# Performance work log

Measured on AMD Instinct MI355X. Metric: run time of the kernel, lower is better.

## Reference

```python
import jax, jax.numpy as jnp
import numpy as np

N_NODES = 50000
N_EDGES = 800000
IN_FEAT = 256
OUT_FEAT = 64
NHEAD = 4
ALPHA = 0.2  # LeakyReLU negative slope


def setup_inputs() -> dict:
    key = jax.random.key(0)
    k_x, k_e, k_w, k_al, k_ar = jax.random.split(key, 5)
    x = jax.random.normal(k_x, (N_NODES, IN_FEAT), dtype=jnp.float32)
    edge = jax.random.randint(k_e, (2, N_EDGES), 0, N_NODES, dtype=jnp.int64)
    # Glorot-uniform style init per reset_parameteres
    stdv_w = np.sqrt(6.0 / (IN_FEAT + OUT_FEAT * NHEAD))
    W = jax.random.uniform(k_w, (IN_FEAT, OUT_FEAT * NHEAD), minval=-stdv_w, maxval=stdv_w, dtype=jnp.float32)
    stdv_a = np.sqrt(6.0 / (NHEAD + OUT_FEAT))
    a_l = jax.random.uniform(k_al, (1, NHEAD, OUT_FEAT), minval=-stdv_a, maxval=stdv_a, dtype=jnp.float32)
    a_r = jax.random.uniform(k_ar, (1, NHEAD, OUT_FEAT), minval=-stdv_a, maxval=stdv_a, dtype=jnp.float32)
    return {"x": x, "edge": edge, "W": W, "a_l": a_l, "a_r": a_r}


def reference(x, edge, W, a_l, a_r):
    # x: [N, Fin], edge: [2, E], W: [Fin, H*F], a_l/a_r: [1, H, F]
    N = x.shape[0]
    H, F = a_l.shape[1], a_l.shape[2]
    h = (x @ W).reshape(N, H, F)                      # [N, H, F]
    h_l = (a_l * h).sum(-1)                            # [N, H]
    h_r = (a_r * h).sum(-1)                            # [N, H]
    row, col = edge[0], edge[1]                        # [E], [E]
    e = jax.nn.leaky_relu(h_l[row] + h_r[col], ALPHA)  # [E, H]
    # segment softmax over edges grouped by target node (row), per head
    m = jax.lax.stop_gradient(jax.ops.segment_max(e, row, num_segments=N))  # [N, H]
    ex = jnp.exp(e - m[row])                           # [E, H]
    denom = jax.ops.segment_sum(ex, row, num_segments=N)[row]  # [E, H]
    att = ex / jnp.maximum(denom, jnp.asarray(1e-16, ex.dtype))
    # spmm scatter-add: out[row] += att * h[col]  (dropout in eval mode = identity)
    msg = att[:, :, None] * h[col]                     # [E, H, F]
    out = jax.ops.segment_sum(msg, row, num_segments=N)  # [N, H, F]
    return out.reshape(N, H * F)                       # concat=True -> [N, H*F]
```

## Files before the change

kernel.cpp:

```cpp
#include <hip/hip_runtime.h>
#include <hip/hip_bf16.h>

#define N_FEAT 256
#define NHEAD 4
#define FDIM 64
#define ALPHA 0.2f

typedef __attribute__((ext_vector_type(8))) short frag8;
typedef __attribute__((ext_vector_type(4))) float f32x4;

static __device__ __forceinline__ unsigned short f2bf(float f) {
    __hip_bfloat16 b = __float2bfloat16(f);
    return *(unsigned short*)&b;
}
static __device__ __forceinline__ float bits2f(unsigned int u) {
    union { unsigned int u; float f; } cv; cv.u = u; return cv.f;
}

__global__ void transpose_w(const float* __restrict__ W, __hip_bfloat16* __restrict__ WT) {
    int n = blockIdx.x;
    int k = threadIdx.x;
    WT[n * 256 + k] = __float2bfloat16(W[k * 256 + n]);
}

__global__ __launch_bounds__(256) void gemm_mfma(const float* __restrict__ x,
                                                 const __hip_bfloat16* __restrict__ WT,
                                                 const float* __restrict__ a_l,
                                                 const float* __restrict__ a_r,
                                                 __hip_bfloat16* __restrict__ h2,
                                                 float* __restrict__ h_l,
                                                 float* __restrict__ h_r, int M) {
    __shared__ __hip_bfloat16 A[64][264];
    const int tid = threadIdx.x;
    const int wave = tid >> 6;
    const int lane = tid & 63;
    const int quad = lane >> 4;
    const int l16 = lane & 15;
    const int row0 = blockIdx.x * 64;

    {
        const int c4 = (tid & 63) * 4;
        const int rb = tid >> 6;
#pragma unroll 4
        for (int pass = 0; pass < 16; ++pass) {
            int r = pass * 4 + rb;
            int gr = row0 + r;
            float4 v = make_float4(0.f, 0.f, 0.f, 0.f);
            if (gr < M) v = *(const float4*)&x[(size_t)gr * 256 + c4];
            unsigned short s[4];
            s[0] = f2bf(v.x); s[1] = f2bf(v.y); s[2] = f2bf(v.z); s[3] = f2bf(v.w);
            *(ushort4*)&A[r][c4] = *(ushort4*)s;
        }
    }
    __syncthreads();

    f32x4 acc[4][4] = {};
    const int kq = quad * 8;
#pragma unroll
    for (int kk = 0; kk < 8; ++kk) {
        frag8 a[4], b[4];
#pragma unroll
        for (int tm = 0; tm < 4; ++tm)
            a[tm] = *(const frag8*)&A[tm * 16 + l16][kk * 32 + kq];
#pragma unroll
        for (int tn = 0; tn < 4; ++tn)
            b[tn] = *(const frag8*)&WT[(size_t)(wave * 64 + tn * 16 + l16) * 256 + kk * 32 + kq];
#pragma unroll
        for (int tm = 0; tm < 4; ++tm)
#pragma unroll
            for (int tn = 0; tn < 4; ++tn)
                acc[tm][tn] = __builtin_amdgcn_mfma_f32_16x16x32_bf16(a[tm], b[tn], acc[tm][tn], 0, 0, 0);
    }

#pragma unroll
    for (int tm = 0; tm < 4; ++tm) {
        int gr_base = row0 + tm * 16 + quad * 4;
#pragma unroll
        for (int tn = 0; tn < 4; ++tn) {
            int colg = wave * 64 + tn * 16 + l16;
#pragma unroll
            for (int reg = 0; reg < 4; ++reg) {
                int gr = gr_base + reg;
                if (gr < M)
                    h2[(size_t)gr * 256 + colg] = __float2bfloat16(acc[tm][tn][reg]);
            }
        }
    }

    float al[4], ar[4];
#pragma unroll
    for (int tn = 0; tn < 4; ++tn) {
        al[tn] = a_l[wave * 64 + tn * 16 + l16];
        ar[tn] = a_r[wave * 64 + tn * 16 + l16];
    }
#pragma unroll
    for (int tm = 0; tm < 4; ++tm) {
#pragma unroll
        for (int reg = 0; reg < 4; ++reg) {
            float vl = 0.f, vr = 0.f;
#pragma unroll
            for (int tn = 0; tn < 4; ++tn) {
                vl += acc[tm][tn][reg] * al[tn];
                vr += acc[tm][tn][reg] * ar[tn];
            }
#pragma unroll
            for (int m = 1; m < 16; m <<= 1) {
                vl += __shfl_xor(vl, m);
                vr += __shfl_xor(vr, m);
            }
            if (l16 == 0) {
                int gr = row0 + tm * 16 + quad * 4 + reg;
                if (gr < M) {
                    h_l[gr * NHEAD + wave] = vl;
                    h_r[gr * NHEAD + wave] = vr;
                }
            }
        }
    }
}

__global__ void hist_kernel(const int* __restrict__ row, int* __restrict__ deg,
                            int* __restrict__ rank, int E) {
    int e = blockIdx.x * blockDim.x + threadIdx.x;
    if (e < E) rank[e] = atomicAdd(&deg[row[e]], 1);
}

__global__ __launch_bounds__(256) void alloc_kernel(const int* __restrict__ deg,
                                                    int* __restrict__ row_ptr,
                                                    int* __restrict__ cursor, int N) {
    int i = blockIdx.x * blockDim.x + threadIdx.x;
    int lane = threadIdx.x & 63;
    int d = (i < N) ? deg[i] : 0;
    int pref = d;
#pragma unroll
    for (int off = 1; off < 64; off <<= 1) {
        int v = __shfl_up(pref, off);
        if (lane >= off) pref += v;
    }
    int total = __shfl(pref, 63);
    int base = 0;
    if (lane == 63) base = atomicAdd(cursor, total);
    base = __shfl(base, 63);
    if (i < N) row_ptr[i] = base + pref - d;
}

__global__ void scatter_kernel(const int* __restrict__ row, const int* __restrict__ col,
                               const int* __restrict__ row_ptr, const int* __restrict__ rank,
                               int* __restrict__ perm_col, int E) {
    int e = blockIdx.x * blockDim.x + threadIdx.x;
    if (e >= E) return;
    perm_col[row_ptr[row[e]] + rank[e]] = col[e];
}

__global__ __launch_bounds__(256) void aggregate_kernel(const __hip_bfloat16* __restrict__ h2,
                                                        const float* __restrict__ h_l,
                                                        const float* __restrict__ h_r,
                                                        const int* __restrict__ row_ptr,
                                                        const int* __restrict__ deg,
                                                        const int* __restrict__ perm_col,
                                                        float* __restrict__ out, int N) {
    int wave = threadIdx.x >> 6;
    int node = blockIdx.x * 4 + wave;
    if (node >= N) return;
    int lane = threadIdx.x & 63;
    int head = lane >> 4;
    int start = row_ptr[node];
    int end = start + deg[node];
    float hl = h_l[node * NHEAD + head];
    const float* hrh = h_r + head;
    const char* hbase = (const char*)h2 + (size_t)lane * 8;

    float4 acc = make_float4(0.f, 0.f, 0.f, 0.f);
    float s = 0.f;
    int j = start;
    for (; j + 4 <= end; j += 4) {
        int c0 = perm_col[j + 0];
        int c1 = perm_col[j + 1];
        int c2 = perm_col[j + 2];
        int c3 = perm_col[j + 3];
        uint2 g0 = *(const uint2*)(hbase + ((size_t)c0 << 9));
        uint2 g1 = *(const uint2*)(hbase + ((size_t)c1 << 9));
        uint2 g2 = *(const uint2*)(hbase + ((size_t)c2 << 9));
        uint2 g3 = *(const uint2*)(hbase + ((size_t)c3 << 9));
        float e0 = hl + hrh[c0 * NHEAD];
        float e1 = hl + hrh[c1 * NHEAD];
        float e2 = hl + hrh[c2 * NHEAD];
        float e3 = hl + hrh[c3 * NHEAD];
        e0 = fmaxf(e0, ALPHA * e0);
        e1 = fmaxf(e1, ALPHA * e1);
        e2 = fmaxf(e2, ALPHA * e2);
        e3 = fmaxf(e3, ALPHA * e3);
        float p0 = __expf(e0), p1 = __expf(e1), p2 = __expf(e2), p3 = __expf(e3);
        acc.x += p0 * bits2f(g0.x << 16);
        acc.y += p0 * bits2f(g0.x & 0xffff0000u);
        acc.z += p0 * bits2f(g0.y << 16);
        acc.w += p0 * bits2f(g0.y & 0xffff0000u);
        s += p0;
        acc.x += p1 * bits2f(g1.x << 16);
        acc.y += p1 * bits2f(g1.x & 0xffff0000u);
        acc.z += p1 * bits2f(g1.y << 16);
        acc.w += p1 * bits2f(g1.y & 0xffff0000u);
        s += p1;
        acc.x += p2 * bits2f(g2.x << 16);
        acc.y += p2 * bits2f(g2.x & 0xffff0000u);
        acc.z += p2 * bits2f(g2.y << 16);
        acc.w += p2 * bits2f(g2.y & 0xffff0000u);
        s += p2;
        acc.x += p3 * bits2f(g3.x << 16);
        acc.y += p3 * bits2f(g3.x & 0xffff0000u);
        acc.z += p3 * bits2f(g3.y << 16);
        acc.w += p3 * bits2f(g3.y & 0xffff0000u);
        s += p3;
    }
    for (; j < end; ++j) {
        int c = perm_col[j];
        uint2 g = *(const uint2*)(hbase + ((size_t)c << 9));
        float e = hl + hrh[c * NHEAD];
        e = fmaxf(e, ALPHA * e);
        float p = __expf(e);
        acc.x += p * bits2f(g.x << 16);
        acc.y += p * bits2f(g.x & 0xffff0000u);
        acc.z += p * bits2f(g.y << 16);
        acc.w += p * bits2f(g.y & 0xffff0000u);
        s += p;
    }
    float inv = 1.f / fmaxf(s, 1e-16f);
    acc.x *= inv; acc.y *= inv; acc.z *= inv; acc.w *= inv;
    *(float4*)&out[(size_t)node * N_FEAT + lane * 4] = acc;
}

extern "C" void kernel_launch(void* const* d_in, const int* in_sizes, int n_in,
                              void* d_out, int out_size, void* d_ws, size_t ws_size,
                              hipStream_t stream) {
    const float* x = (const float*)d_in[0];
    const int* edge = (const int*)d_in[1];
    const float* W = (const float*)d_in[2];
    const float* a_l = (const float*)d_in[3];
    const float* a_r = (const float*)d_in[4];
    float* out = (float*)d_out;

    const int N = in_sizes[0] / N_FEAT;
    const int E = in_sizes[1] / 2;
    const int* row = edge;
    const int* col = edge + E;

    char* p = (char*)d_ws;
    __hip_bfloat16* h2 = (__hip_bfloat16*)p; p += (size_t)N * N_FEAT * sizeof(__hip_bfloat16);
    __hip_bfloat16* WT = (__hip_bfloat16*)p; p += (size_t)256 * 256 * sizeof(__hip_bfloat16);
    float* h_l = (float*)p;      p += (size_t)N * NHEAD * sizeof(float);
    float* h_r = (float*)p;      p += (size_t)N * NHEAD * sizeof(float);
    int* deg = (int*)p;          p += (size_t)(N + 1) * sizeof(int);
    int* row_ptr = (int*)p;      p += (size_t)(N + 4) * sizeof(int);
    int* rank = (int*)p;         p += (size_t)E * sizeof(int);
    int* perm_col = (int*)p;     p += (size_t)E * sizeof(int);
    int* cursor = deg + N;

    hipMemsetAsync(deg, 0, (size_t)(N + 1) * sizeof(int), stream);

    transpose_w<<<256, 256, 0, stream>>>(W, WT);

    gemm_mfma<<<(N + 63) / 64, 256, 0, stream>>>(x, WT, a_l, a_r, h2, h_l, h_r, N);

    hist_kernel<<<(E + 255) / 256, 256, 0, stream>>>(row, deg, rank, E);
    alloc_kernel<<<(N + 255) / 256, 256, 0, stream>>>(deg, row_ptr, cursor, N);
    scatter_kernel<<<(E + 255) / 256, 256, 0, stream>>>(row, col, row_ptr, rank, perm_col, E);

    aggregate_kernel<<<(N + 3) / 4, 256, 0, stream>>>(h2, h_l, h_r, row_ptr, deg, perm_col, out, N);
}
```

Baseline: 270.4 us.

## Stage GEMM output through LDS, compute attention logits via MFMA, pad CSR rows

The GEMM now swaps MFMA operands so each lane holds contiguous output columns. It stages the bf16 result in shared memory and writes h2 with coalesced 16-byte stores instead of scattered 2-byte stores. The a_l/a_r dot products are computed with an extra MFMA on the staged bf16 tile rather than with shuffle reductions, which lowers the precision of the logits. CSR rows are padded to multiples of 4 so the aggregation loop can read column indices with 16-byte vector loads and unroll by 8, at the cost of a larger perm_col workspace.

After: 262.1 us. 3.1% less time.

```diff
diff --git a/kernel.cpp b/kernel.cpp
--- a/kernel.cpp
+++ b/kernel.cpp
@@ -58,62 +58,73 @@
     const int kq = quad * 8;
 #pragma unroll
     for (int kk = 0; kk < 8; ++kk) {
-        frag8 a[4], b[4];
+        frag8 xf[4], wf[4];
 #pragma unroll
         for (int tm = 0; tm < 4; ++tm)
-            a[tm] = *(const frag8*)&A[tm * 16 + l16][kk * 32 + kq];
+            xf[tm] = *(const frag8*)&A[tm * 16 + l16][kk * 32 + kq];
 #pragma unroll
         for (int tn = 0; tn < 4; ++tn)
-            b[tn] = *(const frag8*)&WT[(size_t)(wave * 64 + tn * 16 + l16) * 256 + kk * 32 + kq];
+            wf[tn] = *(const frag8*)&WT[(size_t)(wave * 64 + tn * 16 + l16) * 256 + kk * 32 + kq];
 #pragma unroll
         for (int tm = 0; tm < 4; ++tm)
 #pragma unroll
             for (int tn = 0; tn < 4; ++tn)
-                acc[tm][tn] = __builtin_amdgcn_mfma_f32_16x16x32_bf16(a[tm], b[tn], acc[tm][tn], 0, 0, 0);
-    }
-
+                acc[tm][tn] = __builtin_amdgcn_mfma_f32_16x16x32_bf16(wf[tn], xf[tm], acc[tm][tn], 0, 0, 0);
+    }
+
+    __syncthreads();
+
+#pragma unroll
+    for (int tm = 0; tm < 4; ++tm)
+#pragma unroll
+        for (int tn = 0; tn < 4; ++tn) {
+            unsigned short s4[4];
+            s4[0] = f2bf(acc[tm][tn][0]);
+            s4[1] = f2bf(acc[tm][tn][1]);
+            s4[2] = f2bf(acc[tm][tn][2]);
+            s4[3] = f2bf(acc[tm][tn][3]);
+            *(uint2*)&A[tm * 16 + l16][wave * 64 + tn * 16 + quad * 4] = *(uint2*)s4;
+        }
+    __syncthreads();
+
+    {
+        const int rsub = tid >> 5;
+        const int ce = (tid & 31) * 8;
+#pragma unroll
+        for (int pass = 0; pass < 8; ++pass) {
+            int r = pass * 8 + rsub;
+            int gr = row0 + r;
+            if (gr < M)
+                *(uint4*)&h2[(size_t)gr * 256 + ce] = *(const uint4*)&A[r][ce];
+        }
+    }
+
+    frag8 blr[2];
+#pragma unroll
+    for (int kk = 0; kk < 2; ++kk) {
+#pragma unroll
+        for (int j = 0; j < 8; ++j) {
+            float v = 0.f;
+            int f = wave * 64 + kk * 32 + quad * 8 + j;
+            if (l16 == 0) v = a_l[f];
+            else if (l16 == 1) v = a_r[f];
+            blr[kk][j] = (short)f2bf(v);
+        }
+    }
 #pragma unroll
     for (int tm = 0; tm < 4; ++tm) {
-        int gr_base = row0 + tm * 16 + quad * 4;
-#pragma unroll
-        for (int tn = 0; tn < 4; ++tn) {
-            int colg = wave * 64 + tn * 16 + l16;
-#pragma unroll
-            for (int reg = 0; reg < 4; ++reg) {
-                int gr = gr_base + reg;
-                if (gr < M)
-                    h2[(size_t)gr * 256 + colg] = __float2bfloat16(acc[tm][tn][reg]);
-            }
-        }
-    }
-
-    float al[4], ar[4];
-#pragma unroll
-    for (int tn = 0; tn < 4; ++tn) {
-        al[tn] = a_l[wave * 64 + tn * 16 + l16];
-        ar[tn] = a_r[wave * 64 + tn * 16 + l16];
-    }
-#pragma unroll
-    for (int tm = 0; tm < 4; ++tm) {
+        f32x4 dlr = {0.f, 0.f, 0.f, 0.f};
+#pragma unroll
+        for (int kk = 0; kk < 2; ++kk) {
+            frag8 ah = *(const frag8*)&A[tm * 16 + l16][wave * 64 + kk * 32 + quad * 8];
+            dlr = __builtin_amdgcn_mfma_f32_16x16x32_bf16(ah, blr[kk], dlr, 0, 0, 0);
+        }
 #pragma unroll
         for (int reg = 0; reg < 4; ++reg) {
-            float vl = 0.f, vr = 0.f;
-#pragma unroll
-            for (int tn = 0; tn < 4; ++tn) {
-                vl += acc[tm][tn][reg] * al[tn];
-                vr += acc[tm][tn][reg] * ar[tn];
-            }
-#pragma unroll
-            for (int m = 1; m < 16; m <<= 1) {
-                vl += __shfl_xor(vl, m);
-                vr += __shfl_xor(vr, m);
-            }
-            if (l16 == 0) {
-                int gr = row0 + tm * 16 + quad * 4 + reg;
-                if (gr < M) {
-                    h_l[gr * NHEAD + wave] = vl;
-                    h_r[gr * NHEAD + wave] = vr;
-                }
+            int gr = row0 + tm * 16 + quad * 4 + reg;
+            if (gr < M) {
+                if (l16 == 0) h_l[gr * NHEAD + wave] = dlr[reg];
+                else if (l16 == 1) h_r[gr * NHEAD + wave] = dlr[reg];
             }
         }
     }
@@ -131,7 +142,8 @@
     int i = blockIdx.x * blockDim.x + threadIdx.x;
     int lane = threadIdx.x & 63;
     int d = (i < N) ? deg[i] : 0;
-    int pref = d;
+    int pd = (d + 3) & ~3;
+    int pref = pd;
 #pragma unroll
     for (int off = 1; off < 64; off <<= 1) {
         int v = __shfl_up(pref, off);
@@ -141,7 +153,7 @@
     int base = 0;
     if (lane == 63) base = atomicAdd(cursor, total);
     base = __shfl(base, 63);
-    if (i < N) row_ptr[i] = base + pref - d;
+    if (i < N) row_ptr[i] = base + pref - pd;
 }
 
 __global__ void scatter_kernel(const int* __restrict__ row, const int* __restrict__ col,
@@ -165,7 +177,8 @@
     int lane = threadIdx.x & 63;
     int head = lane >> 4;
     int start = row_ptr[node];
-    int end = start + deg[node];
+    int d = deg[node];
+    int end = start + d;
     float hl = h_l[node * NHEAD + head];
     const float* hrh = h_r + head;
     const char* hbase = (const char*)h2 + (size_t)lane * 8;
@@ -173,44 +186,71 @@
     float4 acc = make_float4(0.f, 0.f, 0.f, 0.f);
     float s = 0.f;
     int j = start;
-    for (; j + 4 <= end; j += 4) {
-        int c0 = perm_col[j + 0];
-        int c1 = perm_col[j + 1];
-        int c2 = perm_col[j + 2];
-        int c3 = perm_col[j + 3];
-        uint2 g0 = *(const uint2*)(hbase + ((size_t)c0 << 9));
-        uint2 g1 = *(const uint2*)(hbase + ((size_t)c1 << 9));
-        uint2 g2 = *(const uint2*)(hbase + ((size_t)c2 << 9));
-        uint2 g3 = *(const uint2*)(hbase + ((size_t)c3 << 9));
-        float e0 = hl + hrh[c0 * NHEAD];
-        float e1 = hl + hrh[c1 * NHEAD];
-        float e2 = hl + hrh[c2 * NHEAD];
-        float e3 = hl + hrh[c3 * NHEAD];
-        e0 = fmaxf(e0, ALPHA * e0);
-        e1 = fmaxf(e1, ALPHA * e1);
-        e2 = fmaxf(e2, ALPHA * e2);
-        e3 = fmaxf(e3, ALPHA * e3);
+    int end8 = start + (d & ~7);
+    for (; j < end8; j += 8) {
+        uint4 q0 = *(const uint4*)&perm_col[j];
+        uint4 q1 = *(const uint4*)&perm_col[j + 4];
+        uint2 g0 = *(const uint2*)(hbase + ((size_t)q0.x << 9));
+        uint2 g1 = *(const uint2*)(hbase + ((size_t)q0.y << 9));
+        uint2 g2 = *(const uint2*)(hbase + ((size_t)q0.z << 9));
+        uint2 g3 = *(const uint2*)(hbase + ((size_t)q0.w << 9));
+        uint2 g4 = *(const uint2*)(hbase + ((size_t)q1.x << 9));
+        uint2 g5 = *(const uint2*)(hbase + ((size_t)q1.y << 9));
+        uint2 g6 = *(const uint2*)(hbase + ((size_t)q1.z << 9));
+        uint2 g7 = *(const uint2*)(hbase + ((size_t)q1.w << 9));
+        float e0 = hl + hrh[q0.x * NHEAD];
+        float e1 = hl + hrh[q0.y * NHEAD];
+        float e2 = hl + hrh[q0.z * NHEAD];
+        float e3 = hl + hrh[q0.w * NHEAD];
+        float e4 = hl + hrh[q1.x * NHEAD];
+        float e5 = hl + hrh[q1.y * NHEAD];
+        float e6 = hl + hrh[q1.z * NHEAD];
+        float e7 = hl + hrh[q1.w * NHEAD];
+        e0 = fmaxf(e0, ALPHA * e0); e1 = fmaxf(e1, ALPHA * e1);
+        e2 = fmaxf(e2, ALPHA * e2); e3 = fmaxf(e3, ALPHA * e3);
+        e4 = fmaxf(e4, ALPHA * e4); e5 = fmaxf(e5, ALPHA * e5);
+        e6 = fmaxf(e6, ALPHA * e6); e7 = fmaxf(e7, ALPHA * e7);
         float p0 = __expf(e0), p1 = __expf(e1), p2 = __expf(e2), p3 = __expf(e3);
-        acc.x += p0 * bits2f(g0.x << 16);
-        acc.y += p0 * bits2f(g0.x & 0xffff0000u);
-        acc.z += p0 * bits2f(g0.y << 16);
-        acc.w += p0 * bits2f(g0.y & 0xffff0000u);
-        s += p0;
-        acc.x += p1 * bits2f(g1.x << 16);
-        acc.y += p1 * bits2f(g1.x & 0xffff0000u);
-        acc.z += p1 * bits2f(g1.y << 16);
-        acc.w += p1 * bits2f(g1.y & 0xffff0000u);
-        s += p1;
-        acc.x += p2 * bits2f(g2.x << 16);
-        acc.y += p2 * bits2f(g2.x & 0xffff0000u);
-        acc.z += p2 * bits2f(g2.y << 16);
-        acc.w += p2 * bits2f(g2.y & 0xffff0000u);
-        s += p2;
-        acc.x += p3 * bits2f(g3.x << 16);
-        acc.y += p3 * bits2f(g3.x & 0xffff0000u);
-        acc.z += p3 * bits2f(g3.y << 16);
-        acc.w += p3 * bits2f(g3.y & 0xffff0000u);
-        s += p3;
+        float p4 = __expf(e4), p5 = __expf(e5), p6 = __expf(e6), p7 = __expf(e7);
+        acc.x += p0 * bits2f(g0.x << 16); acc.y += p0 * bits2f(g0.x & 0xffff0000u);
+        acc.z += p0 * bits2f(g0.y << 16); acc.w += p0 * bits2f(g0.y & 0xffff0000u); s += p0;
+        acc.x += p1 * bits2f(g1.x << 16); acc.y += p1 * bits2f(g1.x & 0xffff0000u);
+        acc.z += p1 * bits2f(g1.y << 16); acc.w += p1 * bits2f(g1.y & 0xffff0000u); s += p1;
+        acc.x += p2 * bits2f(g2.x << 16); acc.y += p2 * bits2f(g2.x & 0xffff0000u);
+        acc.z += p2 * bits2f(g2.y << 16); acc.w += p2 * bits2f(g2.y & 0xffff0000u); s += p2;
+        acc.x += p3 * bits2f(g3.x << 16); acc.y += p3 * bits2f(g3.x & 0xffff0000u);
+        acc.z += p3 * bits2f(g3.y << 16); acc.w += p3 * bits2f(g3.y & 0xffff0000u); s += p3;
+        acc.x += p4 * bits2f(g4.x << 16); acc.y += p4 * bits2f(g4.x & 0xffff0000u);
+        acc.z += p4 * bits2f(g4.y << 16); acc.w += p4 * bits2f(g4.y & 0xffff0000u); s += p4;
+        acc.x += p5 * bits2f(g5.x << 16); acc.y += p5 * bits2f(g5.x & 0xffff0000u);
+        acc.z += p5 * bits2f(g5.y << 16); acc.w += p5 * bits2f(g5.y & 0xffff0000u); s += p5;
+        acc.x += p6 * bits2f(g6.x << 16); acc.y += p6 * bits2f(g6.x & 0xffff0000u);
+        acc.z += p6 * bits2f(g6.y << 16); acc.w += p6 * bits2f(g6.y & 0xffff0000u); s += p6;
+        acc.x += p7 * bits2f(g7.x << 16); acc.y += p7 * bits2f(g7.x & 0xffff0000u);
+        acc.z += p7 * bits2f(g7.y << 16); acc.w += p7 * bits2f(g7.y & 0xffff0000u); s += p7;
+    }
+    if (end - j >= 4) {
+        uint4 q0 = *(const uint4*)&perm_col[j];
+        uint2 g0 = *(const uint2*)(hbase + ((size_t)q0.x << 9));
+        uint2 g1 = *(const uint2*)(hbase + ((size_t)q0.y << 9));
+        uint2 g2 = *(const uint2*)(hbase + ((size_t)q0.z << 9));
+        uint2 g3 = *(const uint2*)(hbase + ((size_t)q0.w << 9));
+        float e0 = hl + hrh[q0.x * NHEAD];
+        float e1 = hl + hrh[q0.y * NHEAD];
+        float e2 = hl + hrh[q0.z * NHEAD];
+        float e3 = hl + hrh[q0.w * NHEAD];
+        e0 = fmaxf(e0, ALPHA * e0); e1 = fmaxf(e1, ALPHA * e1);
+        e2 = fmaxf(e2, ALPHA * e2); e3 = fmaxf(e3, ALPHA * e3);
+        float p0 = __expf(e0), p1 = __expf(e1), p2 = __expf(e2), p3 = __expf(e3);
+        acc.x += p0 * bits2f(g0.x << 16); acc.y += p0 * bits2f(g0.x & 0xffff0000u);
+        acc.z += p0 * bits2f(g0.y << 16); acc.w += p0 * bits2f(g0.y & 0xffff0000u); s += p0;
+        acc.x += p1 * bits2f(g1.x << 16); acc.y += p1 * bits2f(g1.x & 0xffff0000u);
+        acc.z += p1 * bits2f(g1.y << 16); acc.w += p1 * bits2f(g1.y & 0xffff0000u); s += p1;
+        acc.x += p2 * bits2f(g2.x << 16); acc.y += p2 * bits2f(g2.x & 0xffff0000u);
+        acc.z += p2 * bits2f(g2.y << 16); acc.w += p2 * bits2f(g2.y & 0xffff0000u); s += p2;
+        acc.x += p3 * bits2f(g3.x << 16); acc.y += p3 * bits2f(g3.x & 0xffff0000u);
+        acc.z += p3 * bits2f(g3.y << 16); acc.w += p3 * bits2f(g3.y & 0xffff0000u); s += p3;
+        j += 4;
     }
     for (; j < end; ++j) {
         int c = perm_col[j];
@@ -252,7 +292,7 @@
     int* deg = (int*)p;          p += (size_t)(N + 1) * sizeof(int);
     int* row_ptr = (int*)p;      p += (size_t)(N + 4) * sizeof(int);
     int* rank = (int*)p;         p += (size_t)E * sizeof(int);
-    int* perm_col = (int*)p;     p += (size_t)E * sizeof(int);
+    int* perm_col = (int*)p;     p += ((size_t)E + 3 * (size_t)N + 64) * sizeof(int);
     int* cursor = deg + N;
 
     hipMemsetAsync(deg, 0, (size_t)(N + 1) * sizeof(int), stream);
```
